# Kernel tuning notes

Measured on AMD Instinct MI355X. Metric: run time of the kernel, lower is better.

## Reference

```python
import jax, jax.numpy as jnp
import numpy as np
from jax import lax

M0 = 131072      # total atoms
N_ONEHOT = 92    # one-hot width
N_ENV = 55       # env feature width (so 3*(92-19)+55 = 274 -> final flat dim 324)
N_CRYSTALS = 4096


def _conv1d(x, w, b):
    # x: [N, Cin, L], w: [Cout, Cin, K] -> [N, Cout, L-K+1] (VALID, stride 1)
    y = lax.conv_general_dilated(x, w, window_strides=(1,), padding='VALID',
                                 dimension_numbers=('NCH', 'OIH', 'NCH'))
    return y + b[None, :, None]


def _maxpool2(x):
    # MaxPool1d(kernel=2, stride=2) over last dim
    return lax.reduce_window(x, -jnp.inf, lax.max, (1, 1, 2), (1, 1, 2), 'VALID')


def setup_inputs() -> dict:
    key = jax.random.key(0)
    ks = jax.random.split(key, 12)
    inp = {
        'atom_one_hot': jax.random.uniform(ks[0], (M0, N_ONEHOT), jnp.float32),
        'atom_env': jax.random.normal(ks[1], (M0, N_ENV), jnp.float32),
        'crystal_atom_idx': jnp.sort(jax.random.randint(ks[2], (M0,), 0, N_CRYSTALS)),
        'num_segments': N_CRYSTALS,
        # parameters (PyTorch-style fan-in scaled init)
        'conva_w': jax.random.normal(ks[3], (3, 1, 20), jnp.float32) * 0.2,
        'conva_b': jax.random.normal(ks[4], (3,), jnp.float32) * 0.1,
        'conv1_w': jax.random.normal(ks[5], (3, 1, 20), jnp.float32) * 0.2,
        'conv1_b': jax.random.normal(ks[6], (3,), jnp.float32) * 0.1,
        'conv2_w': jax.random.normal(ks[7], (6, 3, 20), jnp.float32) * 0.1,
        'conv2_b': jax.random.normal(ks[8], (6,), jnp.float32) * 0.1,
        'lin_w': jax.random.normal(ks[9], (32, 324), jnp.float32) * 0.05,
        'lin_b': jnp.zeros((32,), jnp.float32),
        'lin1_w': jax.random.normal(ks[10], (1, 32), jnp.float32) * 0.15,
        'lin1_b': jnp.zeros((1,), jnp.float32),
    }
    return inp


def reference(atom_one_hot, atom_env, crystal_atom_idx, num_segments,
              conva_w, conva_b, conv1_w, conv1_b, conv2_w, conv2_b,
              lin_w, lin_b, lin1_w, lin1_b):
    m0 = atom_one_hot.shape[0]
    # per-atom conv over the one-hot vector
    atom = jax.nn.relu(_conv1d(atom_one_hot[:, None, :], conva_w, conva_b))
    atom = atom.reshape(m0, -1)                       # [m0, 3*(n0-19)]
    total = jnp.concatenate([atom, atom_env], axis=1)[:, None, :]  # [m0, 1, 274]
    one = _maxpool2(jax.nn.relu(_conv1d(total, conv1_w, conv1_b)))   # [m0, 3, 127]
    one = _maxpool2(jax.nn.relu(_conv1d(one, conv2_w, conv2_b)))     # [m0, 6, 54]
    one = one.reshape(m0, -1)                          # [m0, 324]
    # ragged per-crystal mean (segment mean) == sum_atom
    sums = jax.ops.segment_sum(one, crystal_atom_idx, num_segments=num_segments)
    counts = jax.ops.segment_sum(jnp.ones((m0,), one.dtype), crystal_atom_idx,
                                 num_segments=num_segments)
    pooled = sums / jnp.maximum(counts, 1.0)[:, None]  # [n_crystals, 324]
    pooled = jax.nn.relu(pooled)
    h = jax.nn.softplus(pooled @ lin_w.T + lin_b)      # [n_crystals, 32]
    return h @ lin1_w.T + lin1_b                       # [n_crystals, 1]
```

## Files before the change

### kernel.cpp

```cpp
#include <hip/hip_runtime.h>
#include <math.h>

#define M0 131072
#define NC 4096
#define FDIM 324
#define APW 4

#define DSWIN21(w0, w1, w2, w3, w4, g, addr)                                   \
  asm volatile("ds_read2_b64 %0, %6 offset0:0 offset1:1\n\t"                   \
               "ds_read2_b64 %1, %6 offset0:2 offset1:3\n\t"                   \
               "ds_read2_b64 %2, %6 offset0:4 offset1:5\n\t"                   \
               "ds_read2_b64 %3, %6 offset0:6 offset1:7\n\t"                   \
               "ds_read2_b64 %4, %6 offset0:8 offset1:9\n\t"                   \
               "ds_read_b32 %5, %6 offset:80\n\t"                              \
               "s_waitcnt lgkmcnt(0)"                                          \
               : "=v"(w0), "=v"(w1), "=v"(w2), "=v"(w3), "=v"(w4), "=v"(g)     \
               : "v"(addr))

#define DSWIN24(w0, w1, w2, w3, w4, w5, addr)                                  \
  asm volatile("ds_read_b128 %0, %6 offset:0\n\t"                              \
               "ds_read_b128 %1, %6 offset:16\n\t"                             \
               "ds_read_b128 %2, %6 offset:32\n\t"                             \
               "ds_read_b128 %3, %6 offset:48\n\t"                             \
               "ds_read_b128 %4, %6 offset:64\n\t"                             \
               "ds_read_b128 %5, %6 offset:80\n\t"                             \
               "s_waitcnt lgkmcnt(0)"                                          \
               : "=v"(w0), "=v"(w1), "=v"(w2), "=v"(w3), "=v"(w4), "=v"(w5)    \
               : "v"(addr))

#define DSWQ5(q, addr)                                                         \
  asm volatile("ds_read_b128 %0, %5 offset:0\n\t"                              \
               "ds_read_b128 %1, %5 offset:16\n\t"                             \
               "ds_read_b128 %2, %5 offset:32\n\t"                             \
               "ds_read_b128 %3, %5 offset:48\n\t"                             \
               "ds_read_b128 %4, %5 offset:64\n\t"                             \
               "s_waitcnt lgkmcnt(0)"                                          \
               : "=v"(q[0]), "=v"(q[1]), "=v"(q[2]), "=v"(q[3]), "=v"(q[4])    \
               : "v"(addr))

#define DSW64(addr, val)  asm volatile("ds_write_b64 %0, %1" :: "v"(addr), "v"(val))
#define DSW32(addr, val)  asm volatile("ds_write_b32 %0, %1" :: "v"(addr), "v"(val))

template<int J>
__device__ __forceinline__ float el21(const float4 (&W)[5], float g) {
    if constexpr (J >= 20) return g;
    else {
        constexpr int q = J >> 2, r = J & 3;
        if constexpr (r == 0) return W[q].x;
        else if constexpr (r == 1) return W[q].y;
        else if constexpr (r == 2) return W[q].z;
        else return W[q].w;
    }
}
template<int J>
__device__ __forceinline__ float el24(const float4 (&W)[6]) {
    constexpr int q = J >> 2, r = J & 3;
    if constexpr (r == 0) return W[q].x;
    else if constexpr (r == 1) return W[q].y;
    else if constexpr (r == 2) return W[q].z;
    else return W[q].w;
}

template<int K0>
__device__ __forceinline__ void fq2(const float4 wq, const float4 (&W)[5], float g,
                                    float& a0, float& a1) {
    a0 = fmaf(el21<K0 + 0>(W, g), wq.x, a0); a1 = fmaf(el21<K0 + 1>(W, g), wq.x, a1);
    a0 = fmaf(el21<K0 + 1>(W, g), wq.y, a0); a1 = fmaf(el21<K0 + 2>(W, g), wq.y, a1);
    a0 = fmaf(el21<K0 + 2>(W, g), wq.z, a0); a1 = fmaf(el21<K0 + 3>(W, g), wq.z, a1);
    a0 = fmaf(el21<K0 + 3>(W, g), wq.w, a0); a1 = fmaf(el21<K0 + 4>(W, g), wq.w, a1);
}
template<int K0>
__device__ __forceinline__ void fq4(const float4 wq, const float4 (&W)[6], float (&a)[4]) {
    a[0] = fmaf(el24<K0 + 0>(W), wq.x, a[0]); a[1] = fmaf(el24<K0 + 1>(W), wq.x, a[1]);
    a[2] = fmaf(el24<K0 + 2>(W), wq.x, a[2]); a[3] = fmaf(el24<K0 + 3>(W), wq.x, a[3]);
    a[0] = fmaf(el24<K0 + 1>(W), wq.y, a[0]); a[1] = fmaf(el24<K0 + 2>(W), wq.y, a[1]);
    a[2] = fmaf(el24<K0 + 3>(W), wq.y, a[2]); a[3] = fmaf(el24<K0 + 4>(W), wq.y, a[3]);
    a[0] = fmaf(el24<K0 + 2>(W), wq.z, a[0]); a[1] = fmaf(el24<K0 + 3>(W), wq.z, a[1]);
    a[2] = fmaf(el24<K0 + 4>(W), wq.z, a[2]); a[3] = fmaf(el24<K0 + 5>(W), wq.z, a[3]);
    a[0] = fmaf(el24<K0 + 3>(W), wq.w, a[0]); a[1] = fmaf(el24<K0 + 4>(W), wq.w, a[1]);
    a[2] = fmaf(el24<K0 + 5>(W), wq.w, a[2]); a[3] = fmaf(el24<K0 + 6>(W), wq.w, a[3]);
}

__global__ __launch_bounds__(256, 8) void atom_kernel(
    const float* __restrict__ oh_g,
    const float* __restrict__ env_g,
    const int*   __restrict__ idx_g,
    const float* __restrict__ wA, const float* __restrict__ bA,
    const float* __restrict__ w1, const float* __restrict__ b1,
    const float* __restrict__ w2, const float* __restrict__ b2,
    float* __restrict__ sums,
    float* __restrict__ counts)
{
    __shared__ __align__(16) float w_lds[480];
    __shared__ __align__(16) float s_total[4][280];
    __shared__ __align__(16) float s_one1[4][384];

    const int bid = (blockIdx.x & 7) * 1024 + (blockIdx.x >> 3);

    const int wave = threadIdx.x >> 6;
    const int lane = threadIdx.x & 63;
    const int tid  = threadIdx.x;

    const unsigned w_b   = (unsigned)(size_t)w_lds;
    const unsigned wD_b  = w_b + 480u;
    const unsigned tot_b = (unsigned)(size_t)&s_total[wave][0];
    const unsigned one_b = (unsigned)(size_t)&s_one1[wave][0];
    const unsigned oh_b  = one_b;

    for (int i = tid; i < 360; i += 256) DSW32(w_b + (120u + (unsigned)i) * 4u, w2[i]);
    if (tid < 60)       DSW32(w_b + (unsigned)tid * 4u, wA[tid]);
    else if (tid < 120) DSW32(w_b + (unsigned)tid * 4u, w1[tid - 60]);
    __syncthreads();

    const int wbase = (bid * 4 + wave) * APW;

    float fa[6] = {0.f, 0.f, 0.f, 0.f, 0.f, 0.f};
    float cnt = 0.f;
    int cur = idx_g[wbase];

    for (int it = 0; it < APW; ++it) {
        const int atom = wbase + it;
        const int cry = idx_g[atom];
        if (cry != cur) {
            if (lane < 54) {
                float* dst = sums + (size_t)cur * FDIM + lane;
                #pragma unroll
                for (int c2 = 0; c2 < 6; ++c2) {
                    atomicAdd(dst + c2 * 54, fa[c2]);
                    fa[c2] = 0.f;
                }
            }
            if (lane == 0) atomicAdd(&counts[cur], cnt);
            cnt = 0.f;
            cur = cry;
        }

        if (lane < 46) {
            const float2 v = *reinterpret_cast<const float2*>(oh_g + (size_t)atom * 92 + 2 * lane);
            DSW64(oh_b + (unsigned)lane * 8u, v);
        }
        if (lane < 55) {
            DSW32(tot_b + (219u + (unsigned)lane) * 4u, env_g[(size_t)atom * 55 + lane]);
        }

        if (lane < 37) {
            float4 W[5]; float g;
            DSWIN21(W[0], W[1], W[2], W[3], W[4], g, oh_b + (unsigned)lane * 8u);
            const unsigned p2 = 2u * (unsigned)lane;
            #pragma unroll
            for (int c = 0; c < 3; ++c) {
                float4 wq[5];
                DSWQ5(wq, w_b + (unsigned)c * 80u);
                float a0 = bA[c], a1 = a0;
                fq2<0>(wq[0], W, g, a0, a1);  fq2<4>(wq[1], W, g, a0, a1);
                fq2<8>(wq[2], W, g, a0, a1);  fq2<12>(wq[3], W, g, a0, a1);
                fq2<16>(wq[4], W, g, a0, a1);
                const unsigned tb = tot_b + (73u * (unsigned)c + p2) * 4u;
                DSW32(tb, fmaxf(a0, 0.f));
                if (p2 + 1 < 73) DSW32(tb + 4u, fmaxf(a1, 0.f));
            }
        }

        {
            float4 W[6];
            DSWIN24(W[0], W[1], W[2], W[3], W[4], W[5], tot_b + (unsigned)lane * 16u);
            #pragma unroll
            for (int c = 0; c < 3; ++c) {
                float4 wq[5];
                DSWQ5(wq, w_b + 240u + (unsigned)c * 80u);
                float a4[4] = {b1[c], b1[c], b1[c], b1[c]};
                fq4<0>(wq[0], W, a4);  fq4<4>(wq[1], W, a4);  fq4<8>(wq[2], W, a4);
                fq4<12>(wq[3], W, a4); fq4<16>(wq[4], W, a4);
                float2 st;
                st.x = fmaxf(fmaxf(a4[0], a4[1]), 0.f);
                st.y = fmaxf(fmaxf(a4[2], a4[3]), 0.f);
                DSW64(one_b + ((unsigned)c * 128u + 2u * (unsigned)lane) * 4u, st);
            }
        }

        if (lane < 54) {
            float acc0[6], acc1[6];
            #pragma unroll
            for (int c2 = 0; c2 < 6; ++c2) { acc0[c2] = b2[c2]; acc1[c2] = acc0[c2]; }
            #pragma unroll
            for (int ch = 0; ch < 3; ++ch) {
                float4 W[5]; float g;
                DSWIN21(W[0], W[1], W[2], W[3], W[4], g,
                        one_b + (unsigned)ch * 512u + (unsigned)lane * 8u);
                #pragma unroll
                for (int c2 = 0; c2 < 6; ++c2) {
                    float4 wq[5];
                    DSWQ5(wq, wD_b + ((unsigned)c2 * 3u + (unsigned)ch) * 80u);
                    fq2<0>(wq[0], W, g, acc0[c2], acc1[c2]);
                    fq2<4>(wq[1], W, g, acc0[c2], acc1[c2]);
                    fq2<8>(wq[2], W, g, acc0[c2], acc1[c2]);
                    fq2<12>(wq[3], W, g, acc0[c2], acc1[c2]);
                    fq2<16>(wq[4], W, g, acc0[c2], acc1[c2]);
                }
            }
            #pragma unroll
            for (int c2 = 0; c2 < 6; ++c2)
                fa[c2] += fmaxf(fmaxf(acc0[c2], acc1[c2]), 0.f);
        }
        cnt += 1.f;
    }

    if (lane < 54) {
        float* dst = sums + (size_t)cur * FDIM + lane;
        #pragma unroll
        for (int c2 = 0; c2 < 6; ++c2) atomicAdd(dst + c2 * 54, fa[c2]);
    }
    if (lane == 0) atomicAdd(&counts[cur], cnt);
}

__global__ __launch_bounds__(64) void head_kernel(
    const float* __restrict__ sums, const float* __restrict__ counts,
    const float* __restrict__ lin_w, const float* __restrict__ lin_b,
    const float* __restrict__ lin1_w, const float* __restrict__ lin1_b,
    float* __restrict__ out)
{
    __shared__ float p[FDIM];
    const int c = blockIdx.x;
    const int lane = threadIdx.x;
    const float inv = 1.0f / fmaxf(counts[c], 1.0f);
    for (int i = lane; i < FDIM; i += 64)
        p[i] = fmaxf(sums[(size_t)c * FDIM + i] * inv, 0.f);
    __syncthreads();

    float r = 0.f;
    if (lane < 32) {
        float acc = lin_b[lane];
        const float* wrow = lin_w + lane * FDIM;
        #pragma unroll 4
        for (int i = 0; i < FDIM; ++i) acc = fmaf(p[i], wrow[i], acc);
        const float sp = (acc > 0.f) ? acc + log1pf(expf(-acc)) : log1pf(expf(acc));
        r = sp * lin1_w[lane];
    }
    #pragma unroll
    for (int off = 16; off; off >>= 1) r += __shfl_down(r, off);
    if (lane == 0) out[c] = r + lin1_b[0];
}

extern "C" void kernel_launch(void* const* d_in, const int* in_sizes, int n_in,
                              void* d_out, int out_size, void* d_ws, size_t ws_size,
                              hipStream_t stream) {
    (void)in_sizes; (void)n_in; (void)out_size; (void)ws_size;
    const float* oh    = (const float*)d_in[0];
    const float* env   = (const float*)d_in[1];
    const int*   idx   = (const int*)  d_in[2];
    const float* wA    = (const float*)d_in[4];
    const float* bA    = (const float*)d_in[5];
    const float* w1    = (const float*)d_in[6];
    const float* b1    = (const float*)d_in[7];
    const float* w2    = (const float*)d_in[8];
    const float* b2    = (const float*)d_in[9];
    const float* lin_w = (const float*)d_in[10];
    const float* lin_b = (const float*)d_in[11];
    const float* lin1_w= (const float*)d_in[12];
    const float* lin1_b= (const float*)d_in[13];

    float* sums   = (float*)d_ws;
    float* counts = sums + (size_t)NC * FDIM;

    hipMemsetAsync(d_ws, 0, ((size_t)NC * FDIM + NC) * sizeof(float), stream);

    atom_kernel<<<M0 / 16, 256, 0, stream>>>(oh, env, idx, wA, bA, w1, b1,
                                             w2, b2, sums, counts);
    head_kernel<<<NC, 64, 0, stream>>>(sums, counts, lin_w, lin_b, lin1_w, lin1_b,
                                       (float*)d_out);
}
```

Baseline: 247.4 us.

## Convert conv inputs and weights to fp16 and use packed fdot2 accumulation

Convolution weights are packed into fp16 pairs in LDS, and each input window is converted to even/odd-shifted fp16 pairs. All three conv stages then use v_dot2 (fdot2) with fp32 accumulation instead of scalar FMAs, which halves the FMA instruction count and shrinks the weight LDS reads. This costs extra conversion instructions and register pressure (occupancy hint lowered from 8 to 6), and fp16 round-toward-zero loses precision relative to the fp32 reference.

```diff
diff --git a/kernel.cpp b/kernel.cpp
--- a/kernel.cpp
+++ b/kernel.cpp
@@ -5,6 +5,22 @@
 #define NC 4096
 #define FDIM 324
 #define APW 4
+
+typedef __attribute__((ext_vector_type(2))) __fp16 h16x2;
+
+#define PKRTZ(a, b) __builtin_amdgcn_cvt_pkrtz((a), (b))
+#if defined(__has_builtin)
+#if __has_builtin(__builtin_amdgcn_fdot2)
+#define FDOT2(a, b, c) __builtin_amdgcn_fdot2((a), (b), (c), false)
+#endif
+#endif
+#ifndef FDOT2
+__device__ __forceinline__ float fdot2f(h16x2 a, h16x2 b, float c) {
+    return (float)a.x * (float)b.x + (float)a.y * (float)b.y + c;
+}
+#define FDOT2(a, b, c) fdot2f((a), (b), (c))
+#endif
+#define BCH(u) __builtin_bit_cast(h16x2, (u))
 
 #define DSWIN21(w0, w1, w2, w3, w4, g, addr)                                   \
   asm volatile("ds_read2_b64 %0, %6 offset0:0 offset1:1\n\t"                   \
@@ -14,7 +30,8 @@
                "ds_read2_b64 %4, %6 offset0:8 offset1:9\n\t"                   \
                "ds_read_b32 %5, %6 offset:80\n\t"                              \
                "s_waitcnt lgkmcnt(0)"                                          \
-               : "=v"(w0), "=v"(w1), "=v"(w2), "=v"(w3), "=v"(w4), "=v"(g)     \
+               : "=&v"(w0), "=&v"(w1), "=&v"(w2), "=&v"(w3), "=&v"(w4),        \
+                 "=&v"(g)                                                      \
                : "v"(addr))
 
 #define DSWIN24(w0, w1, w2, w3, w4, w5, addr)                                  \
@@ -25,17 +42,16 @@
                "ds_read_b128 %4, %6 offset:64\n\t"                             \
                "ds_read_b128 %5, %6 offset:80\n\t"                             \
                "s_waitcnt lgkmcnt(0)"                                          \
-               : "=v"(w0), "=v"(w1), "=v"(w2), "=v"(w3), "=v"(w4), "=v"(w5)    \
+               : "=&v"(w0), "=&v"(w1), "=&v"(w2), "=&v"(w3), "=&v"(w4),        \
+                 "=&v"(w5)                                                     \
                : "v"(addr))
 
-#define DSWQ5(q, addr)                                                         \
-  asm volatile("ds_read_b128 %0, %5 offset:0\n\t"                              \
-               "ds_read_b128 %1, %5 offset:16\n\t"                             \
-               "ds_read_b128 %2, %5 offset:32\n\t"                             \
-               "ds_read_b128 %3, %5 offset:48\n\t"                             \
-               "ds_read_b128 %4, %5 offset:64\n\t"                             \
+#define DSWH10(q0, q1, q2, addr)                                               \
+  asm volatile("ds_read_b128 %0, %3 offset:0\n\t"                              \
+               "ds_read_b128 %1, %3 offset:16\n\t"                             \
+               "ds_read_b64 %2, %3 offset:32\n\t"                              \
                "s_waitcnt lgkmcnt(0)"                                          \
-               : "=v"(q[0]), "=v"(q[1]), "=v"(q[2]), "=v"(q[3]), "=v"(q[4])    \
+               : "=&v"(q0), "=&v"(q1), "=&v"(q2)                               \
                : "v"(addr))
 
 #define DSW64(addr, val)  asm volatile("ds_write_b64 %0, %1" :: "v"(addr), "v"(val))
@@ -61,27 +77,40 @@
     else return W[q].w;
 }
 
-template<int K0>
-__device__ __forceinline__ void fq2(const float4 wq, const float4 (&W)[5], float g,
-                                    float& a0, float& a1) {
-    a0 = fmaf(el21<K0 + 0>(W, g), wq.x, a0); a1 = fmaf(el21<K0 + 1>(W, g), wq.x, a1);
-    a0 = fmaf(el21<K0 + 1>(W, g), wq.y, a0); a1 = fmaf(el21<K0 + 2>(W, g), wq.y, a1);
-    a0 = fmaf(el21<K0 + 2>(W, g), wq.z, a0); a1 = fmaf(el21<K0 + 3>(W, g), wq.z, a1);
-    a0 = fmaf(el21<K0 + 3>(W, g), wq.w, a0); a1 = fmaf(el21<K0 + 4>(W, g), wq.w, a1);
-}
-template<int K0>
-__device__ __forceinline__ void fq4(const float4 wq, const float4 (&W)[6], float (&a)[4]) {
-    a[0] = fmaf(el24<K0 + 0>(W), wq.x, a[0]); a[1] = fmaf(el24<K0 + 1>(W), wq.x, a[1]);
-    a[2] = fmaf(el24<K0 + 2>(W), wq.x, a[2]); a[3] = fmaf(el24<K0 + 3>(W), wq.x, a[3]);
-    a[0] = fmaf(el24<K0 + 1>(W), wq.y, a[0]); a[1] = fmaf(el24<K0 + 2>(W), wq.y, a[1]);
-    a[2] = fmaf(el24<K0 + 3>(W), wq.y, a[2]); a[3] = fmaf(el24<K0 + 4>(W), wq.y, a[3]);
-    a[0] = fmaf(el24<K0 + 2>(W), wq.z, a[0]); a[1] = fmaf(el24<K0 + 3>(W), wq.z, a[1]);
-    a[2] = fmaf(el24<K0 + 4>(W), wq.z, a[2]); a[3] = fmaf(el24<K0 + 5>(W), wq.z, a[3]);
-    a[0] = fmaf(el24<K0 + 3>(W), wq.w, a[0]); a[1] = fmaf(el24<K0 + 4>(W), wq.w, a[1]);
-    a[2] = fmaf(el24<K0 + 5>(W), wq.w, a[2]); a[3] = fmaf(el24<K0 + 6>(W), wq.w, a[3]);
-}
-
-__global__ __launch_bounds__(256, 8) void atom_kernel(
+#define CVT21(ev, od, W, g) do {                                               \
+  ev[0]=PKRTZ(el21<0>(W,g),el21<1>(W,g));   od[0]=PKRTZ(el21<1>(W,g),el21<2>(W,g));   \
+  ev[1]=PKRTZ(el21<2>(W,g),el21<3>(W,g));   od[1]=PKRTZ(el21<3>(W,g),el21<4>(W,g));   \
+  ev[2]=PKRTZ(el21<4>(W,g),el21<5>(W,g));   od[2]=PKRTZ(el21<5>(W,g),el21<6>(W,g));   \
+  ev[3]=PKRTZ(el21<6>(W,g),el21<7>(W,g));   od[3]=PKRTZ(el21<7>(W,g),el21<8>(W,g));   \
+  ev[4]=PKRTZ(el21<8>(W,g),el21<9>(W,g));   od[4]=PKRTZ(el21<9>(W,g),el21<10>(W,g));  \
+  ev[5]=PKRTZ(el21<10>(W,g),el21<11>(W,g)); od[5]=PKRTZ(el21<11>(W,g),el21<12>(W,g)); \
+  ev[6]=PKRTZ(el21<12>(W,g),el21<13>(W,g)); od[6]=PKRTZ(el21<13>(W,g),el21<14>(W,g)); \
+  ev[7]=PKRTZ(el21<14>(W,g),el21<15>(W,g)); od[7]=PKRTZ(el21<15>(W,g),el21<16>(W,g)); \
+  ev[8]=PKRTZ(el21<16>(W,g),el21<17>(W,g)); od[8]=PKRTZ(el21<17>(W,g),el21<18>(W,g)); \
+  ev[9]=PKRTZ(el21<18>(W,g),el21<19>(W,g)); od[9]=PKRTZ(el21<19>(W,g),el21<20>(W,g)); \
+} while (0)
+
+#define CVT24(ev, od, W) do {                                                  \
+  ev[0]=PKRTZ(el24<0>(W),el24<1>(W));   od[0]=PKRTZ(el24<1>(W),el24<2>(W));    \
+  ev[1]=PKRTZ(el24<2>(W),el24<3>(W));   od[1]=PKRTZ(el24<3>(W),el24<4>(W));    \
+  ev[2]=PKRTZ(el24<4>(W),el24<5>(W));   od[2]=PKRTZ(el24<5>(W),el24<6>(W));    \
+  ev[3]=PKRTZ(el24<6>(W),el24<7>(W));   od[3]=PKRTZ(el24<7>(W),el24<8>(W));    \
+  ev[4]=PKRTZ(el24<8>(W),el24<9>(W));   od[4]=PKRTZ(el24<9>(W),el24<10>(W));   \
+  ev[5]=PKRTZ(el24<10>(W),el24<11>(W)); od[5]=PKRTZ(el24<11>(W),el24<12>(W));  \
+  ev[6]=PKRTZ(el24<12>(W),el24<13>(W)); od[6]=PKRTZ(el24<13>(W),el24<14>(W));  \
+  ev[7]=PKRTZ(el24<14>(W),el24<15>(W)); od[7]=PKRTZ(el24<15>(W),el24<16>(W));  \
+  ev[8]=PKRTZ(el24<16>(W),el24<17>(W)); od[8]=PKRTZ(el24<17>(W),el24<18>(W));  \
+  ev[9]=PKRTZ(el24<18>(W),el24<19>(W)); od[9]=PKRTZ(el24<19>(W),el24<20>(W));  \
+  ev[10]=PKRTZ(el24<20>(W),el24<21>(W)); od[10]=PKRTZ(el24<21>(W),el24<22>(W)); \
+} while (0)
+
+#define WPBUILD(wp, q0, q1, q2) do {                                           \
+  wp[0]=BCH(q0.x); wp[1]=BCH(q0.y); wp[2]=BCH(q0.z); wp[3]=BCH(q0.w);          \
+  wp[4]=BCH(q1.x); wp[5]=BCH(q1.y); wp[6]=BCH(q1.z); wp[7]=BCH(q1.w);          \
+  wp[8]=BCH(q2.x); wp[9]=BCH(q2.y);                                            \
+} while (0)
+
+__global__ __launch_bounds__(256, 6) void atom_kernel(
     const float* __restrict__ oh_g,
     const float* __restrict__ env_g,
     const int*   __restrict__ idx_g,
@@ -91,7 +120,7 @@
     float* __restrict__ sums,
     float* __restrict__ counts)
 {
-    __shared__ __align__(16) float w_lds[480];
+    __shared__ __align__(16) float w_lds[288];
     __shared__ __align__(16) float s_total[4][280];
     __shared__ __align__(16) float s_one1[4][384];
 
@@ -102,14 +131,25 @@
     const int tid  = threadIdx.x;
 
     const unsigned w_b   = (unsigned)(size_t)w_lds;
-    const unsigned wD_b  = w_b + 480u;
+    const unsigned wD_b  = w_b + 288u;
     const unsigned tot_b = (unsigned)(size_t)&s_total[wave][0];
     const unsigned one_b = (unsigned)(size_t)&s_one1[wave][0];
     const unsigned oh_b  = one_b;
 
-    for (int i = tid; i < 360; i += 256) DSW32(w_b + (120u + (unsigned)i) * 4u, w2[i]);
-    if (tid < 60)       DSW32(w_b + (unsigned)tid * 4u, wA[tid]);
-    else if (tid < 120) DSW32(w_b + (unsigned)tid * 4u, w1[tid - 60]);
+    if (tid < 30) {
+        const int c = tid / 10, kk = tid % 10;
+        const h16x2 p = PKRTZ(wA[c * 20 + 2 * kk], wA[c * 20 + 2 * kk + 1]);
+        DSW32(w_b + (unsigned)c * 48u + (unsigned)kk * 4u, __builtin_bit_cast(float, p));
+    } else if (tid < 60) {
+        const int t = tid - 30, c = t / 10, kk = t % 10;
+        const h16x2 p = PKRTZ(w1[c * 20 + 2 * kk], w1[c * 20 + 2 * kk + 1]);
+        DSW32(w_b + 144u + (unsigned)c * 48u + (unsigned)kk * 4u, __builtin_bit_cast(float, p));
+    }
+    if (tid >= 64 && tid < 244) {
+        const int j = tid - 64, r = j / 10, kk = j % 10;
+        const h16x2 p = PKRTZ(w2[r * 20 + 2 * kk], w2[r * 20 + 2 * kk + 1]);
+        DSW32(wD_b + (unsigned)r * 48u + (unsigned)kk * 4u, __builtin_bit_cast(float, p));
+    }
     __syncthreads();
 
     const int wbase = (bid * 4 + wave) * APW;
@@ -146,34 +186,49 @@
         if (lane < 37) {
             float4 W[5]; float g;
             DSWIN21(W[0], W[1], W[2], W[3], W[4], g, oh_b + (unsigned)lane * 8u);
+            h16x2 ev[10], od[10];
+            CVT21(ev, od, W, g);
             const unsigned p2 = 2u * (unsigned)lane;
             #pragma unroll
             for (int c = 0; c < 3; ++c) {
-                float4 wq[5];
-                DSWQ5(wq, w_b + (unsigned)c * 80u);
-                float a0 = bA[c], a1 = a0;
-                fq2<0>(wq[0], W, g, a0, a1);  fq2<4>(wq[1], W, g, a0, a1);
-                fq2<8>(wq[2], W, g, a0, a1);  fq2<12>(wq[3], W, g, a0, a1);
-                fq2<16>(wq[4], W, g, a0, a1);
+                uint4 q0, q1; uint2 q2;
+                DSWH10(q0, q1, q2, w_b + (unsigned)c * 48u);
+                h16x2 wp[10];
+                WPBUILD(wp, q0, q1, q2);
+                float e0 = bA[c], e1 = e0;
+                #pragma unroll
+                for (int i = 0; i < 10; ++i) {
+                    e0 = FDOT2(ev[i], wp[i], e0);
+                    e1 = FDOT2(od[i], wp[i], e1);
+                }
                 const unsigned tb = tot_b + (73u * (unsigned)c + p2) * 4u;
-                DSW32(tb, fmaxf(a0, 0.f));
-                if (p2 + 1 < 73) DSW32(tb + 4u, fmaxf(a1, 0.f));
+                DSW32(tb, fmaxf(e0, 0.f));
+                if (p2 + 1 < 73) DSW32(tb + 4u, fmaxf(e1, 0.f));
             }
         }
 
         {
             float4 W[6];
             DSWIN24(W[0], W[1], W[2], W[3], W[4], W[5], tot_b + (unsigned)lane * 16u);
+            h16x2 ev[11], od[11];
+            CVT24(ev, od, W);
             #pragma unroll
             for (int c = 0; c < 3; ++c) {
-                float4 wq[5];
-                DSWQ5(wq, w_b + 240u + (unsigned)c * 80u);
-                float a4[4] = {b1[c], b1[c], b1[c], b1[c]};
-                fq4<0>(wq[0], W, a4);  fq4<4>(wq[1], W, a4);  fq4<8>(wq[2], W, a4);
-                fq4<12>(wq[3], W, a4); fq4<16>(wq[4], W, a4);
+                uint4 q0, q1; uint2 q2;
+                DSWH10(q0, q1, q2, w_b + 144u + (unsigned)c * 48u);
+                h16x2 wp[10];
+                WPBUILD(wp, q0, q1, q2);
+                float a0 = b1[c], a1 = a0, a2 = a0, a3 = a0;
+                #pragma unroll
+                for (int i = 0; i < 10; ++i) {
+                    a0 = FDOT2(ev[i],     wp[i], a0);
+                    a1 = FDOT2(od[i],     wp[i], a1);
+                    a2 = FDOT2(ev[i + 1], wp[i], a2);
+                    a3 = FDOT2(od[i + 1], wp[i], a3);
+                }
                 float2 st;
-                st.x = fmaxf(fmaxf(a4[0], a4[1]), 0.f);
-                st.y = fmaxf(fmaxf(a4[2], a4[3]), 0.f);
+                st.x = fmaxf(fmaxf(a0, a1), 0.f);
+                st.y = fmaxf(fmaxf(a2, a3), 0.f);
                 DSW64(one_b + ((unsigned)c * 128u + 2u * (unsigned)lane) * 4u, st);
             }
         }
@@ -187,15 +242,19 @@
                 float4 W[5]; float g;
                 DSWIN21(W[0], W[1], W[2], W[3], W[4], g,
                         one_b + (unsigned)ch * 512u + (unsigned)lane * 8u);
+                h16x2 ev[10], od[10];
+                CVT21(ev, od, W, g);
                 #pragma unroll
                 for (int c2 = 0; c2 < 6; ++c2) {
-                    float4 wq[5];
-                    DSWQ5(wq, wD_b + ((unsigned)c2 * 3u + (unsigned)ch) * 80u);
-                    fq2<0>(wq[0], W, g, acc0[c2], acc1[c2]);
-                    fq2<4>(wq[1], W, g, acc0[c2], acc1[c2]);
-                    fq2<8>(wq[2], W, g, acc0[c2], acc1[c2]);
-                    fq2<12>(wq[3], W, g, acc0[c2], acc1[c2]);
-                    fq2<16>(wq[4], W, g, acc0[c2], acc1[c2]);
+                    uint4 q0, q1; uint2 q2;
+                    DSWH10(q0, q1, q2, wD_b + ((unsigned)c2 * 3u + (unsigned)ch) * 48u);
+                    h16x2 wp[10];
+                    WPBUILD(wp, q0, q1, q2);
+                    #pragma unroll
+                    for (int i = 0; i < 10; ++i) {
+                        acc0[c2] = FDOT2(ev[i], wp[i], acc0[c2]);
+                        acc1[c2] = FDOT2(od[i], wp[i], acc1[c2]);
+                    }
                 }
             }
             #pragma unroll
```

Result: faster. 210.6 us (median of 2 runs) (-14.9%).
